# Performance work log

Hardware: AMD Instinct MI355X
Metric: run time of the kernel (lower is better)

## Reference

```python
import jax, jax.numpy as jnp
import numpy as np
from jax import lax

B, FMAP, ENC, DEC, ATTN = 64, 512, 256, 512, 256
NUM_CLASSES, MAX_LEN = 96, 30
H, W = 8, 32


def setup_inputs() -> dict:
    key = jax.random.key(0)
    ks = jax.random.split(key, 20)
    s = 0.02
    inp = {
        "feature_map": jax.random.normal(ks[0], (B, FMAP, H, W), jnp.float32),
        "h0": jax.random.normal(ks[1], (2, B, DEC), jnp.float32),
        "c0": jax.random.normal(ks[2], (2, B, DEC), jnp.float32),
        "target": jax.random.randint(ks[3], (B, MAX_LEN), 0, NUM_CLASSES),
        "length": jax.random.randint(ks[4], (B,), 1, MAX_LEN),
        # embedding table: (num_classes+1, enc_dim)
        "emb": jax.random.normal(ks[5], (NUM_CLASSES + 1, ENC), jnp.float32) * s,
        # LSTM layer 0 (input ENC -> DEC), PyTorch gate order i,f,g,o
        "Wih0": jax.random.normal(ks[6], (4 * DEC, ENC), jnp.float32) * s,
        "Whh0": jax.random.normal(ks[7], (4 * DEC, DEC), jnp.float32) * s,
        "bih0": jnp.zeros((4 * DEC,), jnp.float32),
        "bhh0": jnp.zeros((4 * DEC,), jnp.float32),
        # LSTM layer 1 (DEC -> DEC)
        "Wih1": jax.random.normal(ks[8], (4 * DEC, DEC), jnp.float32) * s,
        "Whh1": jax.random.normal(ks[9], (4 * DEC, DEC), jnp.float32) * s,
        "bih1": jnp.zeros((4 * DEC,), jnp.float32),
        "bhh1": jnp.zeros((4 * DEC,), jnp.float32),
        # attention convs: 1x1 on hidden -> linear; 3x3 on fmap; 1x1 attn->1
        "e_lstm_w": jax.random.normal(ks[10], (ATTN, DEC), jnp.float32) * s,
        "e_lstm_b": jnp.zeros((ATTN,), jnp.float32),
        "e_fmap_w": jax.random.normal(ks[11], (ATTN, FMAP, 3, 3), jnp.float32) * s,
        "e_fmap_b": jnp.zeros((ATTN,), jnp.float32),
        "a_w": jax.random.normal(ks[12], (1, ATTN), jnp.float32) * s,
        "a_b": jnp.zeros((1,), jnp.float32),
        # fc: (dec+fmap) -> num_classes+2
        "fc_w": jax.random.normal(ks[13], (NUM_CLASSES + 2, DEC + FMAP), jnp.float32) * s,
        "fc_b": jnp.zeros((NUM_CLASSES + 2,), jnp.float32),
    }
    return inp


def _lstm_cell(x, h, c, Wih, Whh, bih, bhh):
    gates = x @ Wih.T + h @ Whh.T + (bih + bhh)
    i, f, g, o = jnp.split(gates, 4, axis=-1)
    i, f, o = jax.nn.sigmoid(i), jax.nn.sigmoid(f), jax.nn.sigmoid(o)
    c = f * c + i * jnp.tanh(g)
    h = o * jnp.tanh(c)
    return h, c


def reference(feature_map, h0, c0, target, length, emb,
              Wih0, Whh0, bih0, bhh0, Wih1, Whh1, bih1, bhh1,
              e_lstm_w, e_lstm_b, e_fmap_w, e_fmap_b, a_w, a_b, fc_w, fc_b):
    del length  # unused in forward math
    batch = feature_map.shape[0]
    # precompute 3x3 conv on the (constant) feature map once: [B, ATTN, H, W]
    e_fmap = lax.conv_general_dilated(
        feature_map, e_fmap_w, window_strides=(1, 1), padding="SAME",
        dimension_numbers=("NCHW", "OIHW", "NCHW")) + e_fmap_b[None, :, None, None]

    # teacher-forced input sequence: BOS token 0 then target -> [T+1, B]
    labels = jnp.concatenate(
        [jnp.zeros((batch, 1), target.dtype), target], axis=1).T  # [T+1, B]
    emb_seq = emb[labels]  # [T+1, B, ENC]

    def step(carry, x_t):
        h0_, c0_, h1_, c1_ = carry
        h0_, c0_ = _lstm_cell(x_t, h0_, c0_, Wih0, Whh0, bih0, bhh0)
        h1_, c1_ = _lstm_cell(h0_, h1_, c1_, Wih1, Whh1, bih1, bhh1)
        # additive conv attention
        e_h = h1_ @ e_lstm_w.T + e_lstm_b  # [B, ATTN]
        e = jnp.tanh(e_h[:, :, None, None] + e_fmap)  # [B, ATTN, H, W]
        score = jnp.einsum("bahw,a->bhw", e, a_w[0]) + a_b[0]  # [B, H, W]
        a = jax.nn.softmax(score.reshape(batch, -1), axis=-1)
        mask = a.reshape(batch, *score.shape[1:])  # [B, H, W]
        glimpse = jnp.einsum("bchw,bhw->bc", feature_map, mask)  # [B, FMAP]
        logit = jnp.concatenate([h1_, glimpse], axis=-1) @ fc_w.T + fc_b
        return (h0_, c0_, h1_, c1_), (logit, mask, glimpse)

    carry0 = (h0[0], c0[0], h0[1], c0[1])
    _, (logits, masks, glimpses) = lax.scan(step, carry0, emb_seq)
    # time-major -> batch-major
    logits = jnp.transpose(logits, (1, 0, 2))      # [B, T+1, C+2]
    masks = jnp.transpose(masks, (1, 0, 2, 3))     # [B, T+1, H, W]
    glimpses = jnp.transpose(glimpses, (1, 0, 2))  # [B, T+1, FMAP]
    return logits, masks, glimpses
```

## Files before the change

### kernel.cpp

```cpp
#include <hip/hip_runtime.h>
#include <hip/hip_bf16.h>


typedef __bf16 bf16_8 __attribute__((ext_vector_type(8)));
typedef __bf16 bf16_4 __attribute__((ext_vector_type(4)));
typedef __bf16 bf16_2 __attribute__((ext_vector_type(2)));
typedef float f32x4 __attribute__((ext_vector_type(4)));

typedef __hip_bfloat16 bf;

__device__ __forceinline__ float b2f(bf h) { return __bfloat162float(h); }
__device__ __forceinline__ bf f2b(float f) { return __float2bfloat16(f); }
__device__ __forceinline__ float sigm(float x) { return 1.0f / (1.0f + __expf(-x)); }
__device__ __forceinline__ float tanh_f(float x) { return 1.0f - 2.0f / (1.0f + __expf(2.0f * x)); }
__device__ __forceinline__ f32x4 mfma16(bf16_8 a, bf16_8 b, f32x4 c) {
    return __builtin_amdgcn_mfma_f32_16x16x32_bf16(a, b, c, 0, 0, 0);
}

#define NB 64
#define FMAP 512
#define ENC 256
#define DEC 512
#define ATTN 256
#define NC2 98
#define TT 31
#define HW 256
#define PW 34
#define PPOS 340
#define NROWS 1984


__global__ void k_detect(const int* __restrict__ t32, int* __restrict__ flags) {
    __shared__ int i64f;
    int tid = threadIdx.x;
    if (tid == 0) i64f = 1;
    __syncthreads();
    for (int i = tid; i < 960; i += 256)
        if (t32[2 * i + 1] != 0) i64f = 0;
    __syncthreads();
    if (tid == 0) { flags[0] = 0; flags[1] = i64f; }
}

#define N_CVT 17
struct CvtTab {
    const void* src[N_CVT];
    unsigned long long off[N_CVT];
    int n[N_CVT];
};

__global__ void k_cvt(CvtTab tab, unsigned char* __restrict__ ws) {
    int id = blockIdx.y;
    int n = tab.n[id];
    bf* dst = (bf*)(ws + tab.off[id]);
    const float* sf = (const float*)tab.src[id];
    for (int i = blockIdx.x * 256 + threadIdx.x; i < n; i += 256 * gridDim.x)
        dst[i] = f2b(sf[i]);
}


__global__ void k_init_state(const float* __restrict__ h0, const float* __restrict__ c0,
                             bf* __restrict__ h0b, bf* __restrict__ h1_all,
                             float* __restrict__ c0f, float* __restrict__ c1f) {
    int i = blockIdx.x * 256 + threadIdx.x;
    if (i >= NB * DEC) return;
    h0b[32768 + i] = f2b(h0[i]);
    h1_all[i] = f2b(h0[NB * DEC + i]);
    c0f[i] = c0[i];
    c1f[i] = c0[NB * DEC + i];
}

__global__ void k_embed(const int* __restrict__ target, const bf* __restrict__ emb,
                        bf* __restrict__ x_seq, const int* __restrict__ flags) {
    int t = blockIdx.x, b = blockIdx.y, e = threadIdx.x;
    int lab = 0;
    if (t > 0) {
        int idx = b * 30 + (t - 1);
        lab = flags[1] ? target[2 * idx] : target[idx];
    }
    lab = min(max(lab, 0), 96);
    x_seq[(t * NB + b) * ENC + e] = emb[lab * ENC + e];
}

__global__ void k_wt(const bf* __restrict__ ew, bf* __restrict__ wt) {
    int dydx = blockIdx.x, a = blockIdx.y;
    for (int c = threadIdx.x; c < FMAP; c += 256)
        wt[(dydx * ATTN + a) * FMAP + c] = ew[(a * FMAP + c) * 9 + dydx];
}

__global__ void k_zero(unsigned long long* __restrict__ p) {
    p[blockIdx.x * 256 + threadIdx.x] = 0ULL;
}

__global__ __launch_bounds__(256) void k_padT(const float* __restrict__ fmapf,
                                              bf* __restrict__ padT) {
    __shared__ bf T3[64 * 258];
    int b = blockIdx.x, cq = blockIdx.y;
    int tid = threadIdx.x;
    for (int c_l = 0; c_l < 64; c_l++) {
        float v = fmapf[((size_t)(b * FMAP + cq * 64 + c_l)) * HW + tid];
        T3[c_l * 258 + tid] = f2b(v);
    }
    __syncthreads();
    int c_o = tid & 63, pg = tid >> 6;
    for (int it = 0; it < 64; it++) {
        int pos = it * 4 + pg, y = pos >> 5, x = pos & 31;
        padT[((size_t)b * PPOS + (y + 1) * PW + (x + 1)) * FMAP + cq * 64 + c_o] =
            T3[c_o * 258 + pos];
    }
}

__global__ __launch_bounds__(256) void k_conv(const bf* __restrict__ padT,
                                              const bf* __restrict__ wt,
                                              const bf* __restrict__ efb,
                                              bf* __restrict__ ef) {
    __shared__ __align__(16) bf T[257 * 72];
    int b = blockIdx.x, aHalf = blockIdx.y, pHalf = blockIdx.z;
    int tid = threadIdx.x, wv = tid >> 6, lane = tid & 63;
    int q = lane >> 4, l = lane & 15;
    int abase = aHalf * 128 + wv * 32;

    for (int i = tid; i < 72; i += 256) T[256 * 72 + i] = f2b(0.0f);

    const bf* pb = padT + (size_t)b * PPOS * FMAP;
    f32x4 acc[2][8] = {};
    for (int cQ = 0; cQ < 8; cQ++) {
        __syncthreads();
#pragma unroll
        for (int j = 0; j < 8; j++) {
            int chunk = j * 256 + tid;
            int row = chunk >> 3, g = chunk & 7;
            int ppos = 35 + (row >> 5) * PW + (row & 31);
            *(bf16_8*)(T + row * 72 + g * 8) =
                *(const bf16_8*)(pb + (size_t)ppos * FMAP + cQ * 64 + g * 8);
        }
        __syncthreads();
        for (int dydx = 0; dydx < 9; dydx++) {
            int dy = dydx / 3, dx = dydx % 3;
            int rowv[8];
#pragma unroll
            for (int nt = 0; nt < 8; nt++) {
                int y = pHalf * 4 + (nt >> 1);
                int yp = y + dy - 1;
                int x = (nt & 1) * 16 + l;
                int xp = x + dx - 1;
                bool ok = (yp >= 0 && yp < 8 && xp >= 0 && xp < 32);
                rowv[nt] = ok ? (yp * 32 + xp) : 256;
            }
            const bf* wtd = wt + ((size_t)dydx * ATTN) * FMAP;
#pragma unroll
            for (int ck = 0; ck < 2; ck++) {
                int kg = cQ * 64 + ck * 32 + q * 8;
                bf16_8 afr[2];
#pragma unroll
                for (int mt = 0; mt < 2; mt++)
                    afr[mt] = *(const bf16_8*)(wtd + (abase + mt * 16 + l) * FMAP + kg);
#pragma unroll
                for (int nt = 0; nt < 8; nt++) {
                    bf16_8 bfr = *(const bf16_8*)(T + rowv[nt] * 72 + ck * 32 + q * 8);
                    acc[0][nt] = mfma16(afr[0], bfr, acc[0][nt]);
                    acc[1][nt] = mfma16(afr[1], bfr, acc[1][nt]);
                }
            }
        }
    }
#pragma unroll
    for (int mt = 0; mt < 2; mt++)
#pragma unroll
        for (int nt = 0; nt < 8; nt++) {
            int a0 = abase + mt * 16 + q * 4;
            int pos = pHalf * 128 + nt * 16 + l;
            bf16_4 o;
#pragma unroll
            for (int r = 0; r < 4; r++) o[r] = f2b(acc[mt][nt][r] + b2f(efb[a0 + r]));
            *(bf16_4*)(ef + ((size_t)(b * HW + pos)) * ATTN + a0) = o;
        }
}


__global__ __launch_bounds__(256) void k_lstm(
        int s,
        const bf* __restrict__ x_seq,
        const bf* __restrict__ Wih0, const bf* __restrict__ Whh0,
        const bf* __restrict__ bih0, const bf* __restrict__ bhh0,
        const bf* __restrict__ Wih1, const bf* __restrict__ Whh1,
        const bf* __restrict__ bih1, const bf* __restrict__ bhh1,
        bf* __restrict__ h0b, bf* __restrict__ h1_all,
        float* __restrict__ c0f, float* __restrict__ c1f) {
    const int blk = blockIdx.x, tid = threadIdx.x;
    const int wv = tid >> 6, lane = tid & 63;
    const int q = lane >> 4, l = lane & 15;
    const int pcur = s & 1, pprev = (s + 1) & 1;

    if (blk >= 32) {
        if (s > 30) return;
        int d0 = (blk - 32) * 16;
        const bf* xt = x_seq + (size_t)s * NB * ENC;
        const bf* hprev = h0b + pprev * 32768;
        bf* hnew = h0b + pcur * 32768;
        f32x4 acc[4] = {};
        for (int k0 = 0; k0 < ENC; k0 += 32) {
            bf16_8 af = *(const bf16_8*)(xt + (wv * 16 + l) * ENC + k0 + q * 8);
#pragma unroll
            for (int g = 0; g < 4; g++) {
                bf16_8 bfr = *(const bf16_8*)(Wih0 + (g * 512 + d0 + l) * ENC + k0 + q * 8);
                acc[g] = mfma16(af, bfr, acc[g]);
            }
        }
        for (int k0 = 0; k0 < DEC; k0 += 32) {
            bf16_8 af = *(const bf16_8*)(hprev + (wv * 16 + l) * DEC + k0 + q * 8);
#pragma unroll
            for (int g = 0; g < 4; g++) {
                bf16_8 bfr = *(const bf16_8*)(Whh0 + (g * 512 + d0 + l) * DEC + k0 + q * 8);
                acc[g] = mfma16(af, bfr, acc[g]);
            }
        }
        int d = d0 + l;
        float bi[4];
#pragma unroll
        for (int g = 0; g < 4; g++)
            bi[g] = b2f(bih0[g * 512 + d]) + b2f(bhh0[g * 512 + d]);
#pragma unroll
        for (int r = 0; r < 4; r++) {
            int bb = wv * 16 + q * 4 + r;
            float gi = sigm(acc[0][r] + bi[0]);
            float gf = sigm(acc[1][r] + bi[1]);
            float gg = tanh_f(acc[2][r] + bi[2]);
            float go = sigm(acc[3][r] + bi[3]);
            float c = gf * c0f[bb * DEC + d] + gi * gg;
            c0f[bb * DEC + d] = c;
            hnew[bb * DEC + d] = f2b(go * tanh_f(c));
        }
    } else {
        if (s < 1) return;
        int d0 = blk * 16;
        const bf* h0n = h0b + pprev * 32768;
        const bf* h1p = h1_all + (size_t)(s - 1) * 32768;
        bf* h1n = h1_all + (size_t)s * 32768;
        f32x4 acc[4] = {};
        for (int ph = 0; ph < 2; ph++) {
            const bf* Ain = ph ? h1p : h0n;
            const bf* Wp = ph ? Whh1 : Wih1;
            for (int k0 = 0; k0 < DEC; k0 += 32) {
                bf16_8 af = *(const bf16_8*)(Ain + (wv * 16 + l) * DEC + k0 + q * 8);
#pragma unroll
                for (int g = 0; g < 4; g++) {
                    bf16_8 bfr = *(const bf16_8*)(Wp + (g * 512 + d0 + l) * DEC + k0 + q * 8);
                    acc[g] = mfma16(af, bfr, acc[g]);
                }
            }
        }
        int d = d0 + l;
        float bi[4];
#pragma unroll
        for (int g = 0; g < 4; g++)
            bi[g] = b2f(bih1[g * 512 + d]) + b2f(bhh1[g * 512 + d]);
#pragma unroll
        for (int r = 0; r < 4; r++) {
            int bb = wv * 16 + q * 4 + r;
            float gi = sigm(acc[0][r] + bi[0]);
            float gf = sigm(acc[1][r] + bi[1]);
            float gg = tanh_f(acc[2][r] + bi[2]);
            float go = sigm(acc[3][r] + bi[3]);
            float c = gf * c1f[bb * DEC + d] + gi * gg;
            c1f[bb * DEC + d] = c;
            h1n[bb * DEC + d] = f2b(go * tanh_f(c));
        }
    }
}


__global__ __launch_bounds__(256) void k_eh(const bf* __restrict__ h1_all,
                                            const bf* __restrict__ ew,
                                            const bf* __restrict__ eb,
                                            float* __restrict__ EHf) {
    int mtile = blockIdx.x, ntile = blockIdx.y;
    int tid = threadIdx.x, wv = tid >> 6, lane = tid & 63;
    int q = lane >> 4, l = lane & 15;
    const bf* A = h1_all + 32768;
    f32x4 acc[4] = {};
    for (int k0 = 0; k0 < DEC; k0 += 32) {
        bf16_8 af = *(const bf16_8*)(A + (size_t)(mtile * 64 + wv * 16 + l) * DEC + k0 + q * 8);
#pragma unroll
        for (int g = 0; g < 4; g++) {
            bf16_8 bfr = *(const bf16_8*)(ew + (size_t)(ntile * 64 + g * 16 + l) * DEC + k0 + q * 8);
            acc[g] = mfma16(af, bfr, acc[g]);
        }
    }
#pragma unroll
    for (int g = 0; g < 4; g++) {
        int col = ntile * 64 + g * 16 + l;
        float bias = b2f(eb[col]);
#pragma unroll
        for (int r = 0; r < 4; r++) {
            int m = mtile * 64 + wv * 16 + q * 4 + r;
            EHf[(size_t)m * ATTN + col] = acc[g][r] + bias;
        }
    }
}

__global__ __launch_bounds__(256) void k_score(const float* __restrict__ EHf,
                                               const bf* __restrict__ ef,
                                               const bf* __restrict__ a_w,
                                               float* __restrict__ out_masks,
                                               bf* __restrict__ maskb) {
    __shared__ float ehs[4][ATTN];
    __shared__ float aws[ATTN];
    __shared__ float red[256];
    int b = blockIdx.x, tg = blockIdx.y, tid = threadIdx.x;

    aws[tid] = b2f(a_w[tid]);
#pragma unroll
    for (int j = 0; j < 4; j++) {
        int t = tg * 4 + j;
        ehs[j][tid] = (t <= 30) ? EHf[(size_t)(t * NB + b) * ATTN + tid] : 0.0f;
    }
    __syncthreads();

    const bf16_8* er = (const bf16_8*)(ef + ((size_t)b * HW + tid) * ATTN);
    float sj[4] = {0.f, 0.f, 0.f, 0.f};
#pragma unroll 4
    for (int a8 = 0; a8 < ATTN / 8; a8++) {
        bf16_8 e8 = er[a8];
#pragma unroll
        for (int jj = 0; jj < 8; jj++) {
            int a = a8 * 8 + jj;
            float efv = (float)e8[jj];
            float aw = aws[a];
            sj[0] += aw * tanh_f(ehs[0][a] + efv);
            sj[1] += aw * tanh_f(ehs[1][a] + efv);
            sj[2] += aw * tanh_f(ehs[2][a] + efv);
            sj[3] += aw * tanh_f(ehs[3][a] + efv);
        }
    }

#pragma unroll
    for (int j = 0; j < 4; j++) {
        int t = tg * 4 + j;
        red[tid] = sj[j];
        __syncthreads();
        for (int off = 128; off > 0; off >>= 1) {
            if (tid < off) red[tid] = fmaxf(red[tid], red[tid + off]);
            __syncthreads();
        }
        float mx = red[0];
        __syncthreads();
        float ex = __expf(sj[j] - mx);
        red[tid] = ex;
        __syncthreads();
        for (int off = 128; off > 0; off >>= 1) {
            if (tid < off) red[tid] += red[tid + off];
            __syncthreads();
        }
        float mk = ex / red[0];
        __syncthreads();
        if (t <= 30) {
            out_masks[((size_t)b * TT + t) * HW + tid] = mk;
            maskb[((size_t)b * 32 + t) * HW + tid] = f2b(mk);
        } else {
            maskb[((size_t)b * 32 + t) * HW + tid] = f2b(0.0f);
        }
    }
}

__global__ __launch_bounds__(256) void k_glimpse(const float* __restrict__ fmapf,
                                                 const bf* __restrict__ maskb,
                                                 float* __restrict__ out_glimpses,
                                                 bf* __restrict__ glb) {
    int b = blockIdx.x, ctile = blockIdx.y;
    int tid = threadIdx.x, wv = tid >> 6, lane = tid & 63;
    int q = lane >> 4, l = lane & 15;
    const float* A = fmapf + (size_t)b * FMAP * HW + (size_t)(ctile * 64 + wv * 16 + l) * HW;
    const bf* B = maskb + (size_t)b * 32 * HW;
    f32x4 acc[2] = {};
    for (int k0 = 0; k0 < HW; k0 += 32) {
        const float* ap = A + k0 + q * 8;
        f32x4 v0 = *(const f32x4*)(ap);
        f32x4 v1 = *(const f32x4*)(ap + 4);
        bf16_8 af;
#pragma unroll
        for (int j = 0; j < 4; j++) { af[j] = (__bf16)v0[j]; af[4 + j] = (__bf16)v1[j]; }
#pragma unroll
        for (int tt = 0; tt < 2; tt++) {
            bf16_8 bfr = *(const bf16_8*)(B + (size_t)(tt * 16 + l) * HW + k0 + q * 8);
            acc[tt] = mfma16(af, bfr, acc[tt]);
        }
    }
#pragma unroll
    for (int tt = 0; tt < 2; tt++) {
        int t = tt * 16 + l;
        if (t > 30) continue;
#pragma unroll
        for (int r = 0; r < 4; r++) {
            int c = ctile * 64 + wv * 16 + q * 4 + r;
            float g = acc[tt][r];
            out_glimpses[((size_t)b * TT + t) * FMAP + c] = g;
            glb[(size_t)(t * NB + b) * FMAP + c] = f2b(g);
        }
    }
}

__global__ __launch_bounds__(256) void k_logits(const bf* __restrict__ h1_all,
                                                const bf* __restrict__ glb,
                                                const bf* __restrict__ fc_w,
                                                const bf* __restrict__ fc_b,
                                                float* __restrict__ out_logits) {
    int mtile = blockIdx.x, ntile = blockIdx.y;
    int tid = threadIdx.x, wv = tid >> 6, lane = tid & 63;
    int q = lane >> 4, l = lane & 15;
    const bf* A1 = h1_all + 32768;
    int cls = ntile * 16 + l;
    int clsc = min(cls, NC2 - 1);
    int rowA = mtile * 64 + wv * 16 + l;
    f32x4 acc = {};
    for (int k0 = 0; k0 < 1024; k0 += 32) {
        bf16_8 af;
        if (k0 < DEC)
            af = *(const bf16_8*)(A1 + (size_t)rowA * DEC + k0 + q * 8);
        else
            af = *(const bf16_8*)(glb + (size_t)rowA * FMAP + (k0 - DEC) + q * 8);
        bf16_8 bfr = *(const bf16_8*)(fc_w + (size_t)clsc * (DEC + FMAP) + k0 + q * 8);
        acc = mfma16(af, bfr, acc);
    }
    if (cls < NC2) {
        float bias = b2f(fc_b[cls]);
#pragma unroll
        for (int r = 0; r < 4; r++) {
            int m = mtile * 64 + wv * 16 + q * 4 + r;
            int bb = m & 63, t = m >> 6;
            out_logits[((size_t)bb * TT + t) * NC2 + cls] = acc[r] + bias;
        }
    }
}


extern "C" void kernel_launch(void* const* d_in, const int* in_sizes, int n_in,
                              void* d_out, int out_size, void* d_ws, size_t ws_size,
                              hipStream_t stream) {
    float* out = (float*)d_out;
    float* out_logits   = out;
    float* out_masks    = out + 64 * 31 * 98;
    float* out_glimpses = out + 64 * 31 * (98 + 256);

    unsigned char* ws = (unsigned char*)d_ws;
    unsigned long long off = 0;
    auto carve = [&](size_t bytes) {
        unsigned long long o = off;
        off = (off + bytes + 15ULL) & ~15ULL;
        return o;
    };

    unsigned long long o_flags = carve(64);
    static const int cvt_in[N_CVT] = {5, 6, 7, 8, 9, 10, 11, 12, 13, 14, 15, 16, 17, 18, 19, 20, 21};
    static const int cvt_n[N_CVT] = {
        97 * 256, 2048 * 256, 2048 * 512, 2048, 2048,
        2048 * 512, 2048 * 512, 2048, 2048,
        256 * 512, 256, 256 * 512 * 9, 256, 256, 1,
        98 * 1024, 98
    };
    CvtTab tab;
    for (int i = 0; i < N_CVT; i++) {
        tab.src[i] = d_in[cvt_in[i]];
        tab.n[i] = cvt_n[i];
        tab.off[i] = carve((size_t)cvt_n[i] * 2);
    }
    const bf* emb_c    = (const bf*)(ws + tab.off[0]);
    const bf* Wih0_c   = (const bf*)(ws + tab.off[1]);
    const bf* Whh0_c   = (const bf*)(ws + tab.off[2]);
    const bf* bih0_c   = (const bf*)(ws + tab.off[3]);
    const bf* bhh0_c   = (const bf*)(ws + tab.off[4]);
    const bf* Wih1_c   = (const bf*)(ws + tab.off[5]);
    const bf* Whh1_c   = (const bf*)(ws + tab.off[6]);
    const bf* bih1_c   = (const bf*)(ws + tab.off[7]);
    const bf* bhh1_c   = (const bf*)(ws + tab.off[8]);
    const bf* e_lstm_w_c = (const bf*)(ws + tab.off[9]);
    const bf* e_lstm_b_c = (const bf*)(ws + tab.off[10]);
    const bf* e_fmap_w_c = (const bf*)(ws + tab.off[11]);
    const bf* e_fmap_b_c = (const bf*)(ws + tab.off[12]);
    const bf* a_w_c    = (const bf*)(ws + tab.off[13]);
    const bf* fc_w_c   = (const bf*)(ws + tab.off[15]);
    const bf* fc_b_c   = (const bf*)(ws + tab.off[16]);

    bf*    wt     = (bf*)(ws + carve((size_t)9 * 256 * 512 * 2));
    bf*    ef     = (bf*)(ws + carve((size_t)64 * 256 * 256 * 2));
    bf*    x_seq  = (bf*)(ws + carve((size_t)31 * 64 * 256 * 2));
    bf*    h0b    = (bf*)(ws + carve(2 * 65536));
    bf*    h1_all = (bf*)(ws + carve((size_t)32 * 65536));
    float* c0f    = (float*)(ws + carve(131072));
    float* c1f    = (float*)(ws + carve(131072));
    unsigned long long o_padT = carve((size_t)NB * PPOS * FMAP * 2);
    bf*    padT   = (bf*)(ws + o_padT);
    int*   flags  = (int*)(ws + o_flags);

    float* EHf    = (float*)(ws + o_padT);
    bf*    maskb  = (bf*)(ws + o_padT + 2031616ULL);
    bf*    glb    = (bf*)(ws + o_padT + 2031616ULL + 1048576ULL);

    k_detect<<<1, 256, 0, stream>>>((const int*)d_in[3], flags);
    k_cvt<<<dim3(256, N_CVT), 256, 0, stream>>>(tab, ws);
    k_init_state<<<128, 256, 0, stream>>>((const float*)d_in[1], (const float*)d_in[2],
                                          h0b, h1_all, c0f, c1f);
    k_embed<<<dim3(TT, NB), 256, 0, stream>>>((const int*)d_in[3], emb_c, x_seq, flags);
    k_wt<<<dim3(9, ATTN), 256, 0, stream>>>(e_fmap_w_c, wt);
    k_zero<<<10880, 256, 0, stream>>>((unsigned long long*)padT);
    k_padT<<<dim3(NB, 8), 256, 0, stream>>>((const float*)d_in[0], padT);
    k_conv<<<dim3(NB, 2, 2), 256, 0, stream>>>(padT, wt, e_fmap_b_c, ef);

    for (int s = 0; s <= 31; s++)
        k_lstm<<<64, 256, 0, stream>>>(s, x_seq, Wih0_c, Whh0_c, bih0_c, bhh0_c,
                                       Wih1_c, Whh1_c, bih1_c, bhh1_c,
                                       h0b, h1_all, c0f, c1f);

    k_eh<<<dim3(31, 4), 256, 0, stream>>>(h1_all, e_lstm_w_c, e_lstm_b_c, EHf);
    k_score<<<dim3(NB, 8), 256, 0, stream>>>(EHf, ef, a_w_c, out_masks, maskb);
    k_glimpse<<<dim3(NB, 8), 256, 0, stream>>>((const float*)d_in[0], maskb,
                                               out_glimpses, glb);
    k_logits<<<dim3(31, 7), 256, 0, stream>>>(h1_all, glb, fc_w_c, fc_b_c, out_logits);
}
```

Measured before the change: 984.9 us.

## Fuse LSTM timestep launches into a cooperative persistent kernel; retile conv and score

The 32 per-timestep LSTM launches are replaced by one cooperative kernel that loops over timesteps, with a grid-wide sync after each step. This removes per-launch overhead, and the gate biases are loaded once instead of every step. The attention conv now splits positions into quarters, doubling its block count, and the score/softmax kernel handles one timestep per block instead of four, for more parallelism. As a side effect, mask row 31 is no longer zero-filled, and the cooperative grid relies on all 64 blocks being co-resident.

```diff
diff --git a/kernel.cpp b/kernel.cpp
--- a/kernel.cpp
+++ b/kernel.cpp
@@ -1,5 +1,8 @@
 #include <hip/hip_runtime.h>
 #include <hip/hip_bf16.h>
+#include <hip/hip_cooperative_groups.h>
+
+namespace cg = cooperative_groups;
 
 
 typedef __bf16 bf16_8 __attribute__((ext_vector_type(8)));
@@ -114,7 +117,7 @@
                                               const bf* __restrict__ efb,
                                               bf* __restrict__ ef) {
     __shared__ __align__(16) bf T[257 * 72];
-    int b = blockIdx.x, aHalf = blockIdx.y, pHalf = blockIdx.z;
+    int b = blockIdx.x, aHalf = blockIdx.y, pQ = blockIdx.z;
     int tid = threadIdx.x, wv = tid >> 6, lane = tid & 63;
     int q = lane >> 4, l = lane & 15;
     int abase = aHalf * 128 + wv * 32;
@@ -122,7 +125,7 @@
     for (int i = tid; i < 72; i += 256) T[256 * 72 + i] = f2b(0.0f);
 
     const bf* pb = padT + (size_t)b * PPOS * FMAP;
-    f32x4 acc[2][8] = {};
+    f32x4 acc[2][4] = {};
     for (int cQ = 0; cQ < 8; cQ++) {
         __syncthreads();
 #pragma unroll
@@ -136,10 +139,10 @@
         __syncthreads();
         for (int dydx = 0; dydx < 9; dydx++) {
             int dy = dydx / 3, dx = dydx % 3;
-            int rowv[8];
-#pragma unroll
-            for (int nt = 0; nt < 8; nt++) {
-                int y = pHalf * 4 + (nt >> 1);
+            int rowv[4];
+#pragma unroll
+            for (int nt = 0; nt < 4; nt++) {
+                int y = pQ * 2 + (nt >> 1);
                 int yp = y + dy - 1;
                 int x = (nt & 1) * 16 + l;
                 int xp = x + dx - 1;
@@ -155,7 +158,7 @@
                 for (int mt = 0; mt < 2; mt++)
                     afr[mt] = *(const bf16_8*)(wtd + (abase + mt * 16 + l) * FMAP + kg);
 #pragma unroll
-                for (int nt = 0; nt < 8; nt++) {
+                for (int nt = 0; nt < 4; nt++) {
                     bf16_8 bfr = *(const bf16_8*)(T + rowv[nt] * 72 + ck * 32 + q * 8);
                     acc[0][nt] = mfma16(afr[0], bfr, acc[0][nt]);
                     acc[1][nt] = mfma16(afr[1], bfr, acc[1][nt]);
@@ -166,9 +169,9 @@
 #pragma unroll
     for (int mt = 0; mt < 2; mt++)
 #pragma unroll
-        for (int nt = 0; nt < 8; nt++) {
+        for (int nt = 0; nt < 4; nt++) {
             int a0 = abase + mt * 16 + q * 4;
-            int pos = pHalf * 128 + nt * 16 + l;
+            int pos = pQ * 64 + nt * 16 + l;
             bf16_4 o;
 #pragma unroll
             for (int r = 0; r < 4; r++) o[r] = f2b(acc[mt][nt][r] + b2f(efb[a0 + r]));
@@ -177,94 +180,100 @@
 }
 
 
-__global__ __launch_bounds__(256) void k_lstm(
-        int s,
-        const bf* __restrict__ x_seq,
-        const bf* __restrict__ Wih0, const bf* __restrict__ Whh0,
-        const bf* __restrict__ bih0, const bf* __restrict__ bhh0,
-        const bf* __restrict__ Wih1, const bf* __restrict__ Whh1,
-        const bf* __restrict__ bih1, const bf* __restrict__ bhh1,
-        bf* __restrict__ h0b, bf* __restrict__ h1_all,
-        float* __restrict__ c0f, float* __restrict__ c1f) {
+struct SeqArgs {
+    const bf *x_seq, *Wih0, *Whh0, *bih0, *bhh0, *Wih1, *Whh1, *bih1, *bhh1;
+    bf *h0b, *h1_all;
+    float *c0f, *c1f;
+};
+
+__global__ __launch_bounds__(256) void k_seq(SeqArgs A) {
+    cg::grid_group grid = cg::this_grid();
     const int blk = blockIdx.x, tid = threadIdx.x;
     const int wv = tid >> 6, lane = tid & 63;
     const int q = lane >> 4, l = lane & 15;
-    const int pcur = s & 1, pprev = (s + 1) & 1;
-
-    if (blk >= 32) {
-        if (s > 30) return;
-        int d0 = (blk - 32) * 16;
-        const bf* xt = x_seq + (size_t)s * NB * ENC;
-        const bf* hprev = h0b + pprev * 32768;
-        bf* hnew = h0b + pcur * 32768;
-        f32x4 acc[4] = {};
-        for (int k0 = 0; k0 < ENC; k0 += 32) {
-            bf16_8 af = *(const bf16_8*)(xt + (wv * 16 + l) * ENC + k0 + q * 8);
-#pragma unroll
-            for (int g = 0; g < 4; g++) {
-                bf16_8 bfr = *(const bf16_8*)(Wih0 + (g * 512 + d0 + l) * ENC + k0 + q * 8);
-                acc[g] = mfma16(af, bfr, acc[g]);
-            }
-        }
-        for (int k0 = 0; k0 < DEC; k0 += 32) {
-            bf16_8 af = *(const bf16_8*)(hprev + (wv * 16 + l) * DEC + k0 + q * 8);
-#pragma unroll
-            for (int g = 0; g < 4; g++) {
-                bf16_8 bfr = *(const bf16_8*)(Whh0 + (g * 512 + d0 + l) * DEC + k0 + q * 8);
-                acc[g] = mfma16(af, bfr, acc[g]);
-            }
-        }
-        int d = d0 + l;
-        float bi[4];
-#pragma unroll
-        for (int g = 0; g < 4; g++)
-            bi[g] = b2f(bih0[g * 512 + d]) + b2f(bhh0[g * 512 + d]);
-#pragma unroll
-        for (int r = 0; r < 4; r++) {
-            int bb = wv * 16 + q * 4 + r;
-            float gi = sigm(acc[0][r] + bi[0]);
-            float gf = sigm(acc[1][r] + bi[1]);
-            float gg = tanh_f(acc[2][r] + bi[2]);
-            float go = sigm(acc[3][r] + bi[3]);
-            float c = gf * c0f[bb * DEC + d] + gi * gg;
-            c0f[bb * DEC + d] = c;
-            hnew[bb * DEC + d] = f2b(go * tanh_f(c));
-        }
-    } else {
-        if (s < 1) return;
-        int d0 = blk * 16;
-        const bf* h0n = h0b + pprev * 32768;
-        const bf* h1p = h1_all + (size_t)(s - 1) * 32768;
-        bf* h1n = h1_all + (size_t)s * 32768;
-        f32x4 acc[4] = {};
-        for (int ph = 0; ph < 2; ph++) {
-            const bf* Ain = ph ? h1p : h0n;
-            const bf* Wp = ph ? Whh1 : Wih1;
-            for (int k0 = 0; k0 < DEC; k0 += 32) {
-                bf16_8 af = *(const bf16_8*)(Ain + (wv * 16 + l) * DEC + k0 + q * 8);
-#pragma unroll
-                for (int g = 0; g < 4; g++) {
-                    bf16_8 bfr = *(const bf16_8*)(Wp + (g * 512 + d0 + l) * DEC + k0 + q * 8);
-                    acc[g] = mfma16(af, bfr, acc[g]);
+    const bool is0 = (blk >= 32);
+    const int d0 = (is0 ? (blk - 32) : blk) * 16;
+    const int d = d0 + l;
+
+    float bi[4];
+#pragma unroll
+    for (int g = 0; g < 4; g++) {
+        if (is0)
+            bi[g] = b2f(A.bih0[g * 512 + d]) + b2f(A.bhh0[g * 512 + d]);
+        else
+            bi[g] = b2f(A.bih1[g * 512 + d]) + b2f(A.bhh1[g * 512 + d]);
+    }
+
+    for (int s = 0; s <= 31; s++) {
+        const int pcur = s & 1, pprev = (s + 1) & 1;
+        if (is0) {
+            if (s <= 30) {
+                const bf* xt = A.x_seq + (size_t)s * NB * ENC;
+                const bf* hprev = A.h0b + pprev * 32768;
+                bf* hnew = A.h0b + pcur * 32768;
+                f32x4 acc[4] = {};
+                for (int k0 = 0; k0 < ENC; k0 += 32) {
+                    bf16_8 af = *(const bf16_8*)(xt + (wv * 16 + l) * ENC + k0 + q * 8);
+#pragma unroll
+                    for (int g = 0; g < 4; g++) {
+                        bf16_8 bfr = *(const bf16_8*)(A.Wih0 + (g * 512 + d0 + l) * ENC + k0 + q * 8);
+                        acc[g] = mfma16(af, bfr, acc[g]);
+                    }
+                }
+                for (int k0 = 0; k0 < DEC; k0 += 32) {
+                    bf16_8 af = *(const bf16_8*)(hprev + (wv * 16 + l) * DEC + k0 + q * 8);
+#pragma unroll
+                    for (int g = 0; g < 4; g++) {
+                        bf16_8 bfr = *(const bf16_8*)(A.Whh0 + (g * 512 + d0 + l) * DEC + k0 + q * 8);
+                        acc[g] = mfma16(af, bfr, acc[g]);
+                    }
+                }
+#pragma unroll
+                for (int r = 0; r < 4; r++) {
+                    int bb = wv * 16 + q * 4 + r;
+                    float gi = sigm(acc[0][r] + bi[0]);
+                    float gf = sigm(acc[1][r] + bi[1]);
+                    float gg = tanh_f(acc[2][r] + bi[2]);
+                    float go = sigm(acc[3][r] + bi[3]);
+                    float c = gf * A.c0f[bb * DEC + d] + gi * gg;
+                    A.c0f[bb * DEC + d] = c;
+                    hnew[bb * DEC + d] = f2b(go * tanh_f(c));
                 }
             }
-        }
-        int d = d0 + l;
-        float bi[4];
-#pragma unroll
-        for (int g = 0; g < 4; g++)
-            bi[g] = b2f(bih1[g * 512 + d]) + b2f(bhh1[g * 512 + d]);
-#pragma unroll
-        for (int r = 0; r < 4; r++) {
-            int bb = wv * 16 + q * 4 + r;
-            float gi = sigm(acc[0][r] + bi[0]);
-            float gf = sigm(acc[1][r] + bi[1]);
-            float gg = tanh_f(acc[2][r] + bi[2]);
-            float go = sigm(acc[3][r] + bi[3]);
-            float c = gf * c1f[bb * DEC + d] + gi * gg;
-            c1f[bb * DEC + d] = c;
-            h1n[bb * DEC + d] = f2b(go * tanh_f(c));
-        }
+        } else {
+            if (s >= 1) {
+                const bf* h0n = A.h0b + pprev * 32768;
+                const bf* h1p = A.h1_all + (size_t)(s - 1) * 32768;
+                bf* h1n = A.h1_all + (size_t)s * 32768;
+                f32x4 acc[4] = {};
+#pragma unroll
+                for (int ph = 0; ph < 2; ph++) {
+                    const bf* Ain = ph ? h1p : h0n;
+                    const bf* Wp = ph ? A.Whh1 : A.Wih1;
+                    for (int k0 = 0; k0 < DEC; k0 += 32) {
+                        bf16_8 af = *(const bf16_8*)(Ain + (wv * 16 + l) * DEC + k0 + q * 8);
+#pragma unroll
+                        for (int g = 0; g < 4; g++) {
+                            bf16_8 bfr = *(const bf16_8*)(Wp + (g * 512 + d0 + l) * DEC + k0 + q * 8);
+                            acc[g] = mfma16(af, bfr, acc[g]);
+                        }
+                    }
+                }
+#pragma unroll
+                for (int r = 0; r < 4; r++) {
+                    int bb = wv * 16 + q * 4 + r;
+                    float gi = sigm(acc[0][r] + bi[0]);
+                    float gf = sigm(acc[1][r] + bi[1]);
+                    float gg = tanh_f(acc[2][r] + bi[2]);
+                    float go = sigm(acc[3][r] + bi[3]);
+                    float c = gf * A.c1f[bb * DEC + d] + gi * gg;
+                    A.c1f[bb * DEC + d] = c;
+                    h1n[bb * DEC + d] = f2b(go * tanh_f(c));
+                }
+            }
+        }
+        __threadfence();
+        grid.sync();
     }
 }
 
@@ -301,65 +310,52 @@
 __global__ __launch_bounds__(256) void k_score(const float* __restrict__ EHf,
                                                const bf* __restrict__ ef,
                                                const bf* __restrict__ a_w,
+                                               const bf* __restrict__ a_b,
                                                float* __restrict__ out_masks,
                                                bf* __restrict__ maskb) {
-    __shared__ float ehs[4][ATTN];
+    __shared__ float ehs[ATTN];
     __shared__ float aws[ATTN];
     __shared__ float red[256];
-    int b = blockIdx.x, tg = blockIdx.y, tid = threadIdx.x;
-
+    int b = blockIdx.x, t = blockIdx.y, tid = threadIdx.x;
+
+    ehs[tid] = EHf[(size_t)(t * NB + b) * ATTN + tid];
     aws[tid] = b2f(a_w[tid]);
-#pragma unroll
-    for (int j = 0; j < 4; j++) {
-        int t = tg * 4 + j;
-        ehs[j][tid] = (t <= 30) ? EHf[(size_t)(t * NB + b) * ATTN + tid] : 0.0f;
-    }
     __syncthreads();
 
     const bf16_8* er = (const bf16_8*)(ef + ((size_t)b * HW + tid) * ATTN);
-    float sj[4] = {0.f, 0.f, 0.f, 0.f};
+    float s0 = 0.f, s1 = 0.f, s2 = 0.f, s3 = 0.f;
 #pragma unroll 4
     for (int a8 = 0; a8 < ATTN / 8; a8++) {
         bf16_8 e8 = er[a8];
-#pragma unroll
-        for (int jj = 0; jj < 8; jj++) {
-            int a = a8 * 8 + jj;
-            float efv = (float)e8[jj];
-            float aw = aws[a];
-            sj[0] += aw * tanh_f(ehs[0][a] + efv);
-            sj[1] += aw * tanh_f(ehs[1][a] + efv);
-            sj[2] += aw * tanh_f(ehs[2][a] + efv);
-            sj[3] += aw * tanh_f(ehs[3][a] + efv);
-        }
-    }
-
-#pragma unroll
-    for (int j = 0; j < 4; j++) {
-        int t = tg * 4 + j;
-        red[tid] = sj[j];
+        int a = a8 * 8;
+        s0 += aws[a + 0] * tanh_f(ehs[a + 0] + (float)e8[0]);
+        s1 += aws[a + 1] * tanh_f(ehs[a + 1] + (float)e8[1]);
+        s2 += aws[a + 2] * tanh_f(ehs[a + 2] + (float)e8[2]);
+        s3 += aws[a + 3] * tanh_f(ehs[a + 3] + (float)e8[3]);
+        s0 += aws[a + 4] * tanh_f(ehs[a + 4] + (float)e8[4]);
+        s1 += aws[a + 5] * tanh_f(ehs[a + 5] + (float)e8[5]);
+        s2 += aws[a + 6] * tanh_f(ehs[a + 6] + (float)e8[6]);
+        s3 += aws[a + 7] * tanh_f(ehs[a + 7] + (float)e8[7]);
+    }
+    float sc = (s0 + s1) + (s2 + s3) + b2f(a_b[0]);
+    red[tid] = sc;
+    __syncthreads();
+    for (int off = 128; off > 0; off >>= 1) {
+        if (tid < off) red[tid] = fmaxf(red[tid], red[tid + off]);
         __syncthreads();
-        for (int off = 128; off > 0; off >>= 1) {
-            if (tid < off) red[tid] = fmaxf(red[tid], red[tid + off]);
-            __syncthreads();
-        }
-        float mx = red[0];
+    }
+    float mx = red[0];
+    __syncthreads();
+    float ex = __expf(sc - mx);
+    red[tid] = ex;
+    __syncthreads();
+    for (int off = 128; off > 0; off >>= 1) {
+        if (tid < off) red[tid] += red[tid + off];
         __syncthreads();
-        float ex = __expf(sj[j] - mx);
-        red[tid] = ex;
-        __syncthreads();
-        for (int off = 128; off > 0; off >>= 1) {
-            if (tid < off) red[tid] += red[tid + off];
-            __syncthreads();
-        }
-        float mk = ex / red[0];
-        __syncthreads();
-        if (t <= 30) {
-            out_masks[((size_t)b * TT + t) * HW + tid] = mk;
-            maskb[((size_t)b * 32 + t) * HW + tid] = f2b(mk);
-        } else {
-            maskb[((size_t)b * 32 + t) * HW + tid] = f2b(0.0f);
-        }
-    }
+    }
+    float mk = ex / red[0];
+    out_masks[((size_t)b * TT + t) * HW + tid] = mk;
+    maskb[((size_t)b * 32 + t) * HW + tid] = f2b(mk);
 }
 
 __global__ __launch_bounds__(256) void k_glimpse(const float* __restrict__ fmapf,
@@ -477,6 +473,7 @@
     const bf* e_fmap_w_c = (const bf*)(ws + tab.off[11]);
     const bf* e_fmap_b_c = (const bf*)(ws + tab.off[12]);
     const bf* a_w_c    = (const bf*)(ws + tab.off[13]);
+    const bf* a_b_c    = (const bf*)(ws + tab.off[14]);
     const bf* fc_w_c   = (const bf*)(ws + tab.off[15]);
     const bf* fc_b_c   = (const bf*)(ws + tab.off[16]);
 
@@ -503,15 +500,18 @@
     k_wt<<<dim3(9, ATTN), 256, 0, stream>>>(e_fmap_w_c, wt);
     k_zero<<<10880, 256, 0, stream>>>((unsigned long long*)padT);
     k_padT<<<dim3(NB, 8), 256, 0, stream>>>((const float*)d_in[0], padT);
-    k_conv<<<dim3(NB, 2, 2), 256, 0, stream>>>(padT, wt, e_fmap_b_c, ef);
-
-    for (int s = 0; s <= 31; s++)
-        k_lstm<<<64, 256, 0, stream>>>(s, x_seq, Wih0_c, Whh0_c, bih0_c, bhh0_c,
-                                       Wih1_c, Whh1_c, bih1_c, bhh1_c,
-                                       h0b, h1_all, c0f, c1f);
+    k_conv<<<dim3(NB, 2, 4), 256, 0, stream>>>(padT, wt, e_fmap_b_c, ef);
+
+    SeqArgs qa;
+    qa.x_seq = x_seq; qa.Wih0 = Wih0_c; qa.Whh0 = Whh0_c;
+    qa.bih0 = bih0_c; qa.bhh0 = bhh0_c;
+    qa.Wih1 = Wih1_c; qa.Whh1 = Whh1_c; qa.bih1 = bih1_c; qa.bhh1 = bhh1_c;
+    qa.h0b = h0b; qa.h1_all = h1_all; qa.c0f = c0f; qa.c1f = c1f;
+    void* kargs[] = { (void*)&qa };
+    hipLaunchCooperativeKernel((const void*)k_seq, dim3(64), dim3(256), kargs, 0, stream);
 
     k_eh<<<dim3(31, 4), 256, 0, stream>>>(h1_all, e_lstm_w_c, e_lstm_b_c, EHf);
-    k_score<<<dim3(NB, 8), 256, 0, stream>>>(EHf, ef, a_w_c, out_masks, maskb);
+    k_score<<<dim3(NB, TT), 256, 0, stream>>>(EHf, ef, a_w_c, a_b_c, out_masks, maskb);
     k_glimpse<<<dim3(NB, 8), 256, 0, stream>>>((const float*)d_in[0], maskb,
                                                out_glimpses, glb);
     k_logits<<<dim3(31, 7), 256, 0, stream>>>(h1_all, glb, fc_w_c, fc_b_c, out_logits);
```

Result: slower. 1.576 ms (+60.0%).

## Split LSTM K across waves, drop padded fmap, widen conv and score grids

Applied to the files above, without the earlier changes.

The LSTM step kernel now runs 8 waves per block. Each half of the waves handles one part of the K reduction (input or recurrent weights), and the partial sums are combined through shared memory, shortening the serial per-step latency. The padded transposed feature map and its zeroing kernel are removed, since conv bounds already map out-of-range positions to a zero row. The conv grid is split into quarters of positions so twice as many blocks run. The score kernel now handles one timestep per block instead of four, which adds parallelism but re-reads the conv features more often. It also no longer writes the padding row 31 of the bf16 mask buffer, so that row keeps whatever was left in the aliased workspace.

```diff
diff --git a/kernel.cpp b/kernel.cpp
--- a/kernel.cpp
+++ b/kernel.cpp
@@ -25,8 +25,6 @@
 #define NC2 98
 #define TT 31
 #define HW 256
-#define PW 34
-#define PPOS 340
 #define NROWS 1984
 
 
@@ -87,12 +85,8 @@
         wt[(dydx * ATTN + a) * FMAP + c] = ew[(a * FMAP + c) * 9 + dydx];
 }
 
-__global__ void k_zero(unsigned long long* __restrict__ p) {
-    p[blockIdx.x * 256 + threadIdx.x] = 0ULL;
-}
-
 __global__ __launch_bounds__(256) void k_padT(const float* __restrict__ fmapf,
-                                              bf* __restrict__ padT) {
+                                              bf* __restrict__ fmapT) {
     __shared__ bf T3[64 * 258];
     int b = blockIdx.x, cq = blockIdx.y;
     int tid = threadIdx.x;
@@ -103,43 +97,41 @@
     __syncthreads();
     int c_o = tid & 63, pg = tid >> 6;
     for (int it = 0; it < 64; it++) {
-        int pos = it * 4 + pg, y = pos >> 5, x = pos & 31;
-        padT[((size_t)b * PPOS + (y + 1) * PW + (x + 1)) * FMAP + cq * 64 + c_o] =
-            T3[c_o * 258 + pos];
-    }
-}
-
-__global__ __launch_bounds__(256) void k_conv(const bf* __restrict__ padT,
+        int pos = it * 4 + pg;
+        fmapT[((size_t)b * HW + pos) * FMAP + cq * 64 + c_o] = T3[c_o * 258 + pos];
+    }
+}
+
+__global__ __launch_bounds__(256) void k_conv(const bf* __restrict__ fmapT,
                                               const bf* __restrict__ wt,
                                               const bf* __restrict__ efb,
                                               bf* __restrict__ ef) {
     __shared__ __align__(16) bf T[257 * 72];
-    int b = blockIdx.x, aHalf = blockIdx.y, pHalf = blockIdx.z;
+    int b = blockIdx.x, aHalf = blockIdx.y, pQ = blockIdx.z;
     int tid = threadIdx.x, wv = tid >> 6, lane = tid & 63;
     int q = lane >> 4, l = lane & 15;
     int abase = aHalf * 128 + wv * 32;
 
     for (int i = tid; i < 72; i += 256) T[256 * 72 + i] = f2b(0.0f);
 
-    const bf* pb = padT + (size_t)b * PPOS * FMAP;
-    f32x4 acc[2][8] = {};
+    const bf* pb = fmapT + (size_t)b * HW * FMAP;
+    f32x4 acc[2][4] = {};
     for (int cQ = 0; cQ < 8; cQ++) {
         __syncthreads();
 #pragma unroll
         for (int j = 0; j < 8; j++) {
             int chunk = j * 256 + tid;
             int row = chunk >> 3, g = chunk & 7;
-            int ppos = 35 + (row >> 5) * PW + (row & 31);
             *(bf16_8*)(T + row * 72 + g * 8) =
-                *(const bf16_8*)(pb + (size_t)ppos * FMAP + cQ * 64 + g * 8);
+                *(const bf16_8*)(pb + (size_t)row * FMAP + cQ * 64 + g * 8);
         }
         __syncthreads();
         for (int dydx = 0; dydx < 9; dydx++) {
             int dy = dydx / 3, dx = dydx % 3;
-            int rowv[8];
-#pragma unroll
-            for (int nt = 0; nt < 8; nt++) {
-                int y = pHalf * 4 + (nt >> 1);
+            int rowv[4];
+#pragma unroll
+            for (int nt = 0; nt < 4; nt++) {
+                int y = pQ * 2 + (nt >> 1);
                 int yp = y + dy - 1;
                 int x = (nt & 1) * 16 + l;
                 int xp = x + dx - 1;
@@ -155,7 +147,7 @@
                 for (int mt = 0; mt < 2; mt++)
                     afr[mt] = *(const bf16_8*)(wtd + (abase + mt * 16 + l) * FMAP + kg);
 #pragma unroll
-                for (int nt = 0; nt < 8; nt++) {
+                for (int nt = 0; nt < 4; nt++) {
                     bf16_8 bfr = *(const bf16_8*)(T + rowv[nt] * 72 + ck * 32 + q * 8);
                     acc[0][nt] = mfma16(afr[0], bfr, acc[0][nt]);
                     acc[1][nt] = mfma16(afr[1], bfr, acc[1][nt]);
@@ -166,9 +158,9 @@
 #pragma unroll
     for (int mt = 0; mt < 2; mt++)
 #pragma unroll
-        for (int nt = 0; nt < 8; nt++) {
+        for (int nt = 0; nt < 4; nt++) {
             int a0 = abase + mt * 16 + q * 4;
-            int pos = pHalf * 128 + nt * 16 + l;
+            int pos = pQ * 64 + nt * 16 + l;
             bf16_4 o;
 #pragma unroll
             for (int r = 0; r < 4; r++) o[r] = f2b(acc[mt][nt][r] + b2f(efb[a0 + r]));
@@ -177,7 +169,7 @@
 }
 
 
-__global__ __launch_bounds__(256) void k_lstm(
+__global__ __launch_bounds__(512) void k_lstm(
         int s,
         const bf* __restrict__ x_seq,
         const bf* __restrict__ Wih0, const bf* __restrict__ Whh0,
@@ -186,84 +178,104 @@
         const bf* __restrict__ bih1, const bf* __restrict__ bhh1,
         bf* __restrict__ h0b, bf* __restrict__ h1_all,
         float* __restrict__ c0f, float* __restrict__ c1f) {
+    __shared__ f32x4 red4[4][4][64];
     const int blk = blockIdx.x, tid = threadIdx.x;
-    const int wv = tid >> 6, lane = tid & 63;
+    const int wave = tid >> 6, lane = tid & 63;
     const int q = lane >> 4, l = lane & 15;
+    const int kh = wave >> 2, bt = wave & 3;
     const int pcur = s & 1, pprev = (s + 1) & 1;
-
-    if (blk >= 32) {
+    const bool is0 = (blk >= 32);
+    const int d0 = (is0 ? (blk - 32) : blk) * 16;
+    const int d = d0 + l;
+
+    f32x4 acc[4] = {};
+    if (is0) {
         if (s > 30) return;
-        int d0 = (blk - 32) * 16;
         const bf* xt = x_seq + (size_t)s * NB * ENC;
         const bf* hprev = h0b + pprev * 32768;
-        bf* hnew = h0b + pcur * 32768;
-        f32x4 acc[4] = {};
-        for (int k0 = 0; k0 < ENC; k0 += 32) {
-            bf16_8 af = *(const bf16_8*)(xt + (wv * 16 + l) * ENC + k0 + q * 8);
+        if (kh == 0) {
+#pragma unroll
+            for (int k0 = 0; k0 < ENC; k0 += 32) {
+                bf16_8 af = *(const bf16_8*)(xt + (bt * 16 + l) * ENC + k0 + q * 8);
+#pragma unroll
+                for (int g = 0; g < 4; g++) {
+                    bf16_8 bfr = *(const bf16_8*)(Wih0 + (g * 512 + d0 + l) * ENC + k0 + q * 8);
+                    acc[g] = mfma16(af, bfr, acc[g]);
+                }
+            }
+        } else {
+#pragma unroll 4
+            for (int k0 = 0; k0 < DEC; k0 += 32) {
+                bf16_8 af = *(const bf16_8*)(hprev + (bt * 16 + l) * DEC + k0 + q * 8);
+#pragma unroll
+                for (int g = 0; g < 4; g++) {
+                    bf16_8 bfr = *(const bf16_8*)(Whh0 + (g * 512 + d0 + l) * DEC + k0 + q * 8);
+                    acc[g] = mfma16(af, bfr, acc[g]);
+                }
+            }
+#pragma unroll
+            for (int g = 0; g < 4; g++) red4[bt][g][lane] = acc[g];
+        }
+        __syncthreads();
+        if (kh == 0) {
+            bf* hnew = h0b + pcur * 32768;
+            float bi[4];
 #pragma unroll
             for (int g = 0; g < 4; g++) {
-                bf16_8 bfr = *(const bf16_8*)(Wih0 + (g * 512 + d0 + l) * ENC + k0 + q * 8);
-                acc[g] = mfma16(af, bfr, acc[g]);
-            }
-        }
-        for (int k0 = 0; k0 < DEC; k0 += 32) {
-            bf16_8 af = *(const bf16_8*)(hprev + (wv * 16 + l) * DEC + k0 + q * 8);
-#pragma unroll
-            for (int g = 0; g < 4; g++) {
-                bf16_8 bfr = *(const bf16_8*)(Whh0 + (g * 512 + d0 + l) * DEC + k0 + q * 8);
-                acc[g] = mfma16(af, bfr, acc[g]);
-            }
-        }
-        int d = d0 + l;
-        float bi[4];
-#pragma unroll
-        for (int g = 0; g < 4; g++)
-            bi[g] = b2f(bih0[g * 512 + d]) + b2f(bhh0[g * 512 + d]);
-#pragma unroll
-        for (int r = 0; r < 4; r++) {
-            int bb = wv * 16 + q * 4 + r;
-            float gi = sigm(acc[0][r] + bi[0]);
-            float gf = sigm(acc[1][r] + bi[1]);
-            float gg = tanh_f(acc[2][r] + bi[2]);
-            float go = sigm(acc[3][r] + bi[3]);
-            float c = gf * c0f[bb * DEC + d] + gi * gg;
-            c0f[bb * DEC + d] = c;
-            hnew[bb * DEC + d] = f2b(go * tanh_f(c));
+                acc[g] += red4[bt][g][lane];
+                bi[g] = b2f(bih0[g * 512 + d]) + b2f(bhh0[g * 512 + d]);
+            }
+#pragma unroll
+            for (int r = 0; r < 4; r++) {
+                int bb = bt * 16 + q * 4 + r;
+                float gi = sigm(acc[0][r] + bi[0]);
+                float gf = sigm(acc[1][r] + bi[1]);
+                float gg = tanh_f(acc[2][r] + bi[2]);
+                float go = sigm(acc[3][r] + bi[3]);
+                float c = gf * c0f[bb * DEC + d] + gi * gg;
+                c0f[bb * DEC + d] = c;
+                hnew[bb * DEC + d] = f2b(go * tanh_f(c));
+            }
         }
     } else {
         if (s < 1) return;
-        int d0 = blk * 16;
         const bf* h0n = h0b + pprev * 32768;
         const bf* h1p = h1_all + (size_t)(s - 1) * 32768;
-        bf* h1n = h1_all + (size_t)s * 32768;
-        f32x4 acc[4] = {};
-        for (int ph = 0; ph < 2; ph++) {
-            const bf* Ain = ph ? h1p : h0n;
-            const bf* Wp = ph ? Whh1 : Wih1;
-            for (int k0 = 0; k0 < DEC; k0 += 32) {
-                bf16_8 af = *(const bf16_8*)(Ain + (wv * 16 + l) * DEC + k0 + q * 8);
-#pragma unroll
-                for (int g = 0; g < 4; g++) {
-                    bf16_8 bfr = *(const bf16_8*)(Wp + (g * 512 + d0 + l) * DEC + k0 + q * 8);
-                    acc[g] = mfma16(af, bfr, acc[g]);
-                }
-            }
-        }
-        int d = d0 + l;
-        float bi[4];
-#pragma unroll
-        for (int g = 0; g < 4; g++)
-            bi[g] = b2f(bih1[g * 512 + d]) + b2f(bhh1[g * 512 + d]);
-#pragma unroll
-        for (int r = 0; r < 4; r++) {
-            int bb = wv * 16 + q * 4 + r;
-            float gi = sigm(acc[0][r] + bi[0]);
-            float gf = sigm(acc[1][r] + bi[1]);
-            float gg = tanh_f(acc[2][r] + bi[2]);
-            float go = sigm(acc[3][r] + bi[3]);
-            float c = gf * c1f[bb * DEC + d] + gi * gg;
-            c1f[bb * DEC + d] = c;
-            h1n[bb * DEC + d] = f2b(go * tanh_f(c));
+        const bf* Ain = kh ? h1p : h0n;
+        const bf* Wp  = kh ? Whh1 : Wih1;
+#pragma unroll 4
+        for (int k0 = 0; k0 < DEC; k0 += 32) {
+            bf16_8 af = *(const bf16_8*)(Ain + (bt * 16 + l) * DEC + k0 + q * 8);
+#pragma unroll
+            for (int g = 0; g < 4; g++) {
+                bf16_8 bfr = *(const bf16_8*)(Wp + (g * 512 + d0 + l) * DEC + k0 + q * 8);
+                acc[g] = mfma16(af, bfr, acc[g]);
+            }
+        }
+        if (kh == 1) {
+#pragma unroll
+            for (int g = 0; g < 4; g++) red4[bt][g][lane] = acc[g];
+        }
+        __syncthreads();
+        if (kh == 0) {
+            bf* h1n = h1_all + (size_t)s * 32768;
+            float bi[4];
+#pragma unroll
+            for (int g = 0; g < 4; g++) {
+                acc[g] += red4[bt][g][lane];
+                bi[g] = b2f(bih1[g * 512 + d]) + b2f(bhh1[g * 512 + d]);
+            }
+#pragma unroll
+            for (int r = 0; r < 4; r++) {
+                int bb = bt * 16 + q * 4 + r;
+                float gi = sigm(acc[0][r] + bi[0]);
+                float gf = sigm(acc[1][r] + bi[1]);
+                float gg = tanh_f(acc[2][r] + bi[2]);
+                float go = sigm(acc[3][r] + bi[3]);
+                float c = gf * c1f[bb * DEC + d] + gi * gg;
+                c1f[bb * DEC + d] = c;
+                h1n[bb * DEC + d] = f2b(go * tanh_f(c));
+            }
         }
     }
 }
@@ -303,63 +315,49 @@
                                                const bf* __restrict__ a_w,
                                                float* __restrict__ out_masks,
                                                bf* __restrict__ maskb) {
-    __shared__ float ehs[4][ATTN];
+    __shared__ float ehs[ATTN];
     __shared__ float aws[ATTN];
     __shared__ float red[256];
-    int b = blockIdx.x, tg = blockIdx.y, tid = threadIdx.x;
-
+    int b = blockIdx.x, t = blockIdx.y, tid = threadIdx.x;
+
+    ehs[tid] = EHf[(size_t)(t * NB + b) * ATTN + tid];
     aws[tid] = b2f(a_w[tid]);
-#pragma unroll
-    for (int j = 0; j < 4; j++) {
-        int t = tg * 4 + j;
-        ehs[j][tid] = (t <= 30) ? EHf[(size_t)(t * NB + b) * ATTN + tid] : 0.0f;
-    }
     __syncthreads();
 
     const bf16_8* er = (const bf16_8*)(ef + ((size_t)b * HW + tid) * ATTN);
-    float sj[4] = {0.f, 0.f, 0.f, 0.f};
+    float s0 = 0.f, s1 = 0.f, s2 = 0.f, s3 = 0.f;
 #pragma unroll 4
     for (int a8 = 0; a8 < ATTN / 8; a8++) {
         bf16_8 e8 = er[a8];
-#pragma unroll
-        for (int jj = 0; jj < 8; jj++) {
-            int a = a8 * 8 + jj;
-            float efv = (float)e8[jj];
-            float aw = aws[a];
-            sj[0] += aw * tanh_f(ehs[0][a] + efv);
-            sj[1] += aw * tanh_f(ehs[1][a] + efv);
-            sj[2] += aw * tanh_f(ehs[2][a] + efv);
-            sj[3] += aw * tanh_f(ehs[3][a] + efv);
-        }
-    }
-
-#pragma unroll
-    for (int j = 0; j < 4; j++) {
-        int t = tg * 4 + j;
-        red[tid] = sj[j];
+        int a = a8 * 8;
+        s0 += aws[a + 0] * tanh_f(ehs[a + 0] + (float)e8[0]);
+        s1 += aws[a + 1] * tanh_f(ehs[a + 1] + (float)e8[1]);
+        s2 += aws[a + 2] * tanh_f(ehs[a + 2] + (float)e8[2]);
+        s3 += aws[a + 3] * tanh_f(ehs[a + 3] + (float)e8[3]);
+        s0 += aws[a + 4] * tanh_f(ehs[a + 4] + (float)e8[4]);
+        s1 += aws[a + 5] * tanh_f(ehs[a + 5] + (float)e8[5]);
+        s2 += aws[a + 6] * tanh_f(ehs[a + 6] + (float)e8[6]);
+        s3 += aws[a + 7] * tanh_f(ehs[a + 7] + (float)e8[7]);
+    }
+    float sc = (s0 + s1) + (s2 + s3);
+    red[tid] = sc;
+    __syncthreads();
+    for (int off = 128; off > 0; off >>= 1) {
+        if (tid < off) red[tid] = fmaxf(red[tid], red[tid + off]);
         __syncthreads();
-        for (int off = 128; off > 0; off >>= 1) {
-            if (tid < off) red[tid] = fmaxf(red[tid], red[tid + off]);
-            __syncthreads();
-        }
-        float mx = red[0];
+    }
+    float mx = red[0];
+    __syncthreads();
+    float ex = __expf(sc - mx);
+    red[tid] = ex;
+    __syncthreads();
+    for (int off = 128; off > 0; off >>= 1) {
+        if (tid < off) red[tid] += red[tid + off];
         __syncthreads();
-        float ex = __expf(sj[j] - mx);
-        red[tid] = ex;
-        __syncthreads();
-        for (int off = 128; off > 0; off >>= 1) {
-            if (tid < off) red[tid] += red[tid + off];
-            __syncthreads();
-        }
-        float mk = ex / red[0];
-        __syncthreads();
-        if (t <= 30) {
-            out_masks[((size_t)b * TT + t) * HW + tid] = mk;
-            maskb[((size_t)b * 32 + t) * HW + tid] = f2b(mk);
-        } else {
-            maskb[((size_t)b * 32 + t) * HW + tid] = f2b(0.0f);
-        }
-    }
+    }
+    float mk = ex / red[0];
+    out_masks[((size_t)b * TT + t) * HW + tid] = mk;
+    maskb[((size_t)b * 32 + t) * HW + tid] = f2b(mk);
 }
 
 __global__ __launch_bounds__(256) void k_glimpse(const float* __restrict__ fmapf,
@@ -487,13 +485,13 @@
     bf*    h1_all = (bf*)(ws + carve((size_t)32 * 65536));
     float* c0f    = (float*)(ws + carve(131072));
     float* c1f    = (float*)(ws + carve(131072));
-    unsigned long long o_padT = carve((size_t)NB * PPOS * FMAP * 2);
-    bf*    padT   = (bf*)(ws + o_padT);
+    unsigned long long o_fmapT = carve((size_t)NB * HW * FMAP * 2);
+    bf*    fmapT  = (bf*)(ws + o_fmapT);
     int*   flags  = (int*)(ws + o_flags);
 
-    float* EHf    = (float*)(ws + o_padT);
-    bf*    maskb  = (bf*)(ws + o_padT + 2031616ULL);
-    bf*    glb    = (bf*)(ws + o_padT + 2031616ULL + 1048576ULL);
+    float* EHf    = (float*)(ws + o_fmapT);
+    bf*    maskb  = (bf*)(ws + o_fmapT + 2031616ULL);
+    bf*    glb    = (bf*)(ws + o_fmapT + 2031616ULL + 1048576ULL);
 
     k_detect<<<1, 256, 0, stream>>>((const int*)d_in[3], flags);
     k_cvt<<<dim3(256, N_CVT), 256, 0, stream>>>(tab, ws);
@@ -501,17 +499,16 @@
                                           h0b, h1_all, c0f, c1f);
     k_embed<<<dim3(TT, NB), 256, 0, stream>>>((const int*)d_in[3], emb_c, x_seq, flags);
     k_wt<<<dim3(9, ATTN), 256, 0, stream>>>(e_fmap_w_c, wt);
-    k_zero<<<10880, 256, 0, stream>>>((unsigned long long*)padT);
-    k_padT<<<dim3(NB, 8), 256, 0, stream>>>((const float*)d_in[0], padT);
-    k_conv<<<dim3(NB, 2, 2), 256, 0, stream>>>(padT, wt, e_fmap_b_c, ef);
+    k_padT<<<dim3(NB, 8), 256, 0, stream>>>((const float*)d_in[0], fmapT);
+    k_conv<<<dim3(NB, 2, 4), 256, 0, stream>>>(fmapT, wt, e_fmap_b_c, ef);
 
     for (int s = 0; s <= 31; s++)
-        k_lstm<<<64, 256, 0, stream>>>(s, x_seq, Wih0_c, Whh0_c, bih0_c, bhh0_c,
+        k_lstm<<<64, 512, 0, stream>>>(s, x_seq, Wih0_c, Whh0_c, bih0_c, bhh0_c,
                                        Wih1_c, Whh1_c, bih1_c, bhh1_c,
                                        h0b, h1_all, c0f, c1f);
 
     k_eh<<<dim3(31, 4), 256, 0, stream>>>(h1_all, e_lstm_w_c, e_lstm_b_c, EHf);
-    k_score<<<dim3(NB, 8), 256, 0, stream>>>(EHf, ef, a_w_c, out_masks, maskb);
+    k_score<<<dim3(NB, TT), 256, 0, stream>>>(EHf, ef, a_w_c, out_masks, maskb);
     k_glimpse<<<dim3(NB, 8), 256, 0, stream>>>((const float*)d_in[0], maskb,
                                                out_glimpses, glb);
     k_logits<<<dim3(31, 7), 256, 0, stream>>>(h1_all, glb, fc_w_c, fc_b_c, out_logits);
```

After: 994.7 us. No clear change (+1.0%).
